# Performance work log

Measured on AMD Instinct MI355X. Metric: run time of the kernel, lower is better.

Reference implementation:

```python
import jax, jax.numpy as jnp
import numpy as np

B, T, V, C, H, HS, L, DFF = 8192, 8, 65, 512, 8, 64, 6, 2048
LN_EPS = 1e-5


def _layernorm(x, g, b):
    mu = jnp.mean(x, axis=-1, keepdims=True)
    var = jnp.mean(jnp.square(x - mu), axis=-1, keepdims=True)
    return (x - mu) * jax.lax.rsqrt(var + LN_EPS) * g + b


def setup_inputs() -> dict:
    key = jax.random.key(0)
    ks = jax.random.split(key, 16)
    s = 0.02
    inp = {
        "idx": jax.random.randint(ks[0], (B, T), 0, V),
        "tok_table": jax.random.normal(ks[1], (V, C), jnp.float32) * s,
        "pos_table": jax.random.normal(ks[2], (T, C), jnp.float32) * s,
        "wq": jax.random.normal(ks[3], (L, H, C, HS), jnp.float32) * s,
        "wk": jax.random.normal(ks[4], (L, H, C, HS), jnp.float32) * s,
        "wv": jax.random.normal(ks[5], (L, H, C, HS), jnp.float32) * s,
        "proj_w": jax.random.normal(ks[6], (L, C, C), jnp.float32) * s,
        "proj_b": jnp.zeros((L, C), jnp.float32),
        "w1": jax.random.normal(ks[7], (L, C, DFF), jnp.float32) * s,
        "b1": jnp.zeros((L, DFF), jnp.float32),
        "w2": jax.random.normal(ks[8], (L, DFF, C), jnp.float32) * s,
        "b2": jnp.zeros((L, C), jnp.float32),
        "ln1_g": jnp.ones((L, C), jnp.float32),
        "ln1_b": jnp.zeros((L, C), jnp.float32),
        "ln2_g": jnp.ones((L, C), jnp.float32),
        "ln2_b": jnp.zeros((L, C), jnp.float32),
        "lm_w": jax.random.normal(ks[9], (C, V), jnp.float32) * s,
        "lm_b": jnp.zeros((V,), jnp.float32),
    }
    return inp


def reference(idx, tok_table, pos_table, wq, wk, wv, proj_w, proj_b,
              w1, b1, w2, b2, ln1_g, ln1_b, ln2_g, ln2_b, lm_w, lm_b):
    idx = idx[:, -T:]
    x = tok_table[idx] + pos_table[None, :T, :]  # [B,T,C]
    mask = jnp.tril(jnp.ones((T, T), bool))
    scale = C ** (-0.5)  # NOTE: original scales by n_embed, not head_size
    for l in range(L):
        q = jnp.einsum('btc,hcd->bhtd', x, wq[l])
        k = jnp.einsum('btc,hcd->bhtd', x, wk[l])
        v = jnp.einsum('btc,hcd->bhtd', x, wv[l])
        att = jnp.einsum('bhtd,bhsd->bhts', q, k) * scale
        att = jnp.where(mask, att, -jnp.inf)
        att = jax.nn.softmax(att, axis=-1)
        o = jnp.einsum('bhts,bhsd->bhtd', att, v)
        o = o.transpose(0, 2, 1, 3).reshape(x.shape[0], T, C)  # concat heads
        o = o @ proj_w[l] + proj_b[l]
        x = _layernorm(x + o, ln1_g[l], ln1_b[l])  # post-norm
        h = jax.nn.relu(x @ w1[l] + b1[l]) @ w2[l] + b2[l]
        x = _layernorm(x + h, ln2_g[l], ln2_b[l])
    logits = x @ lm_w + lm_b  # [B,T,V]
    return logits
```

## Files before the change

### kernel.cpp

```cpp
#include <hip/hip_runtime.h>
#include <hip/hip_bf16.h>
#include <math.h>

#define NTOK  65536
#define CDIM  512
#define NHEAD 8
#define HSZ   64
#define NLAYER 6
#define DFF   2048
#define VOCAB 65

typedef unsigned short u16;
typedef __attribute__((ext_vector_type(8))) __bf16 bf16x8;
typedef __attribute__((ext_vector_type(4))) float f32x4;
typedef __attribute__((ext_vector_type(8))) unsigned short ushort8;

__device__ __forceinline__ float b2f(u16 u) {
    union { unsigned int i; float f; } x; x.i = ((unsigned int)u) << 16; return x.f;
}
__device__ __forceinline__ u16 f2b(float f) {
    union { float f; unsigned int i; } x; x.f = f;
    unsigned int r = x.i + 0x7fffu + ((x.i >> 16) & 1u);
    return (u16)(r >> 16);
}

__device__ __forceinline__ void async16(const u16* g, u16* l) {
    __builtin_amdgcn_global_load_lds(
        (const __attribute__((address_space(1))) void*)g,
        (__attribute__((address_space(3))) void*)l, 16, 0, 0);
}

template<int EPI>
__global__ __launch_bounds__(512)
void gemm_bt(const u16* __restrict__ A, const u16* __restrict__ Bt,
             void* __restrict__ Cout, const float* __restrict__ bias,
             const u16* __restrict__ res, int K, int N, int Nout)
{
    __shared__ u16 lA[2 * 256 * 32];
    __shared__ u16 lB[2 * 128 * 32];
    const int tid  = threadIdx.x;

    const int Nx = gridDim.x;
    const int id = blockIdx.y * Nx + blockIdx.x;
    const int xcd = id & 7;
    const int j0  = id >> 3;
    const int mt  = xcd + 8 * (j0 / Nx);
    const int nt  = j0 - (j0 / Nx) * Nx;
    const int m0  = mt * 256;
    const int n0  = nt * 128;

    const int lane = tid & 63;
    const int wv   = tid >> 6;
    const int wr   = (wv >> 1) * 64;
    const int wc   = (wv & 1) * 64;
    const int r16  = lane & 15;
    const int quad = lane >> 4;

    f32x4 acc[4][4] = {};

    const int srow = tid >> 2, skseg = (tid & 3) * 8;
    const u16* pA  = A  + (size_t)(m0 + srow) * K + skseg;
    const u16* pA2 = pA + (size_t)128 * K;
    const u16* pB  = Bt + (size_t)(n0 + srow) * K + skseg;
    u16* lAt = &lA[(size_t)tid * 8];
    u16* lBt = &lB[(size_t)tid * 8];

    async16(pA,  lAt);
    async16(pA2, lAt + 4096);
    async16(pB,  lBt);
    __syncthreads();

    int s = 0;
    for (int k0 = 0; k0 < K; k0 += 32) {
        if (k0 + 32 < K) {
            const int sn = (s ^ 1);
            async16(pA  + k0 + 32, lAt + sn * 8192);
            async16(pA2 + k0 + 32, lAt + sn * 8192 + 4096);
            async16(pB  + k0 + 32, lBt + sn * 4096);
        }
        const u16* bA = &lA[s * 8192];
        const u16* bB = &lB[s * 4096];
        bf16x8 af[4], bfr[4];
#pragma unroll
        for (int i = 0; i < 4; i++)
            af[i] = *(const bf16x8*)(const void*)&bA[(wr + i * 16 + r16) * 32 + quad * 8];
#pragma unroll
        for (int j = 0; j < 4; j++)
            bfr[j] = *(const bf16x8*)(const void*)&bB[(wc + j * 16 + r16) * 32 + quad * 8];
#pragma unroll
        for (int j = 0; j < 4; j++)
#pragma unroll
            for (int i = 0; i < 4; i++)
                acc[j][i] = __builtin_amdgcn_mfma_f32_16x16x32_bf16(bfr[j], af[i], acc[j][i], 0, 0, 0);
        __syncthreads();
        s ^= 1;
    }

#pragma unroll
    for (int i = 0; i < 4; i++) {
        const int row = m0 + wr + i * 16 + r16;
#pragma unroll
        for (int j = 0; j < 4; j++) {
            const int colb = n0 + wc + j * 16 + quad * 4;
            float v[4];
#pragma unroll
            for (int r = 0; r < 4; r++) v[r] = acc[j][i][r];
            if (EPI == 1 || EPI == 2) {
                const f32x4 b4 = *(const f32x4*)(const void*)&bias[colb];
#pragma unroll
                for (int r = 0; r < 4; r++) v[r] += b4[r];
            }
            if (EPI == 1) {
                const uint2 rv = *(const uint2*)(const void*)&res[(size_t)row * N + colb];
                v[0] += b2f((u16)(rv.x & 0xffffu));
                v[1] += b2f((u16)(rv.x >> 16));
                v[2] += b2f((u16)(rv.y & 0xffffu));
                v[3] += b2f((u16)(rv.y >> 16));
            }
            if (EPI == 2) {
#pragma unroll
                for (int r = 0; r < 4; r++) v[r] = fmaxf(v[r], 0.f);
            }
            if (EPI == 3) {
#pragma unroll
                for (int r = 0; r < 4; r++) {
                    const int col = colb + r;
                    if (col < Nout)
                        ((float*)Cout)[(size_t)row * Nout + col] = v[r] + bias[col];
                }
            } else {
                uint2 o;
                o.x = (unsigned)f2b(v[0]) | ((unsigned)f2b(v[1]) << 16);
                o.y = (unsigned)f2b(v[2]) | ((unsigned)f2b(v[3]) << 16);
                *(uint2*)(void*)&((u16*)Cout)[(size_t)row * N + colb] = o;
            }
        }
    }
}

__global__ __launch_bounds__(256)
void attn_k(const u16* __restrict__ qkv, u16* __restrict__ out)
{
    __shared__ float sq[4][8][64], sk[4][8][64], sv[4][8][64], sp[4][64];
    const int w = threadIdx.x >> 6, lane = threadIdx.x & 63;
    const int unit = blockIdx.x * 4 + w;
    const int b = unit >> 3, h = unit & 7;
    const size_t base = (size_t)b * 8 * 1536 + h * 64;
#pragma unroll
    for (int t = 0; t < 8; t++) {
        sq[w][t][lane] = b2f(qkv[base + t * 1536 + lane]);
        sk[w][t][lane] = b2f(qkv[base + t * 1536 + 512 + lane]);
        sv[w][t][lane] = b2f(qkv[base + t * 1536 + 1024 + lane]);
    }
    __syncthreads();
    const int t = lane >> 3, s = lane & 7;
    float sc = -1e30f;
    if (s <= t) {
        float d = 0.f;
#pragma unroll
        for (int c = 0; c < 64; c++) d += sq[w][t][c] * sk[w][s][c];
        sc = d * 0.04419417382415922f;
    }
    float mx = sc;
#pragma unroll
    for (int m = 1; m < 8; m <<= 1) mx = fmaxf(mx, __shfl_xor(mx, m, 8));
    float e = __expf(sc - mx);
    if (s > t) e = 0.f;
    float sum = e;
#pragma unroll
    for (int m = 1; m < 8; m <<= 1) sum += __shfl_xor(sum, m, 8);
    sp[w][lane] = e / sum;
    __syncthreads();
#pragma unroll
    for (int tt = 0; tt < 8; tt++) {
        float a = 0.f;
#pragma unroll
        for (int ss = 0; ss < 8; ss++) a += sp[w][tt * 8 + ss] * sv[w][ss][lane];
        out[((size_t)b * 8 + tt) * 512 + h * 64 + lane] = f2b(a);
    }
}

__global__ __launch_bounds__(256)
void ln_k(const u16* __restrict__ y, const float* __restrict__ g,
          const float* __restrict__ be, u16* __restrict__ x)
{
    const int w = threadIdx.x >> 6, lane = threadIdx.x & 63;
    const size_t tok = (size_t)blockIdx.x * 4 + w;
    const u16* row = y + tok * 512 + lane * 8;
    ushort8 raw = *(const ushort8*)(const void*)row;
    float v[8];
#pragma unroll
    for (int i = 0; i < 8; i++) v[i] = b2f(raw[i]);
    float s = 0.f;
#pragma unroll
    for (int i = 0; i < 8; i++) s += v[i];
#pragma unroll
    for (int m = 1; m < 64; m <<= 1) s += __shfl_xor(s, m, 64);
    const float mu = s * (1.f / 512.f);
    float q = 0.f;
#pragma unroll
    for (int i = 0; i < 8; i++) { float d = v[i] - mu; q += d * d; }
#pragma unroll
    for (int m = 1; m < 64; m <<= 1) q += __shfl_xor(q, m, 64);
    const float inv = rsqrtf(q * (1.f / 512.f) + 1e-5f);
    f32x4 g0  = *(const f32x4*)(const void*)&g[lane * 8];
    f32x4 g1  = *(const f32x4*)(const void*)&g[lane * 8 + 4];
    f32x4 b0  = *(const f32x4*)(const void*)&be[lane * 8];
    f32x4 b1v = *(const f32x4*)(const void*)&be[lane * 8 + 4];
    ushort8 o;
#pragma unroll
    for (int i = 0; i < 4; i++) o[i]     = f2b((v[i] - mu) * inv * g0[i] + b0[i]);
#pragma unroll
    for (int i = 0; i < 4; i++) o[i + 4] = f2b((v[i + 4] - mu) * inv * g1[i] + b1v[i]);
    *(ushort8*)(void*)&x[tok * 512 + lane * 8] = o;
}

__global__ __launch_bounds__(256)
void embed_k(const int* __restrict__ idx, const float* __restrict__ tokt,
             const float* __restrict__ pos, u16* __restrict__ xb)
{
    const int tk = blockIdx.x;
    const int t = tk & 7;
    const int ix = idx[tk];
    const int c = threadIdx.x;
    const size_t o = (size_t)tk * 512;
    xb[o + c]       = f2b(tokt[(size_t)ix * 512 + c]       + pos[t * 512 + c]);
    xb[o + c + 256] = f2b(tokt[(size_t)ix * 512 + c + 256] + pos[t * 512 + c + 256]);
}

__global__ __launch_bounds__(256)
void conv_t2_k(const float* __restrict__ in, u16* __restrict__ out, int K, int N)
{
    __shared__ float t[32][33];
    const int tx = threadIdx.x & 31, ty4 = (threadIdx.x >> 5) * 4;
    const int n0 = blockIdx.x * 32, k0 = blockIdx.y * 32, l = blockIdx.z;
    const size_t per = (size_t)K * N;
    const float* src = in + l * per;
#pragma unroll
    for (int r = 0; r < 4; r++)
        t[ty4 + r][tx] = src[(size_t)(k0 + ty4 + r) * N + n0 + tx];
    __syncthreads();
    u16* dst = out + l * per;
#pragma unroll
    for (int r = 0; r < 4; r++)
        dst[(size_t)(n0 + ty4 + r) * K + k0 + tx] = f2b(t[tx][ty4 + r]);
}

__global__ __launch_bounds__(256)
void conv_qkv2_k(const float* __restrict__ wq, const float* __restrict__ wk,
                 const float* __restrict__ wv, u16* __restrict__ out)
{
    __shared__ float t[32][33];
    const int tx = threadIdx.x & 31, ty4 = (threadIdx.x >> 5) * 4;
    const int c0 = blockIdx.x * 32, d0 = blockIdx.y * 32;
    const int z = blockIdx.z;
    const int sel = z / 48, rem = z - sel * 48;
    const int l = rem >> 3, h = rem & 7;
    const float* src = (sel == 0) ? wq : (sel == 1) ? wk : wv;
    const float* sb = src + (((size_t)l * 8 + h) * 512) * 64;
#pragma unroll
    for (int r = 0; r < 4; r++)
        t[ty4 + r][tx] = sb[(size_t)(c0 + ty4 + r) * 64 + d0 + tx];
    __syncthreads();
    u16* dst = out + (size_t)l * 786432 + (size_t)(sel * 512 + h * 64 + d0) * 512;
#pragma unroll
    for (int r = 0; r < 4; r++)
        dst[(size_t)(ty4 + r) * 512 + c0 + tx] = f2b(t[tx][ty4 + r]);
}

__global__ __launch_bounds__(256)
void conv_lm_k(const float* __restrict__ lm_w, u16* __restrict__ out)
{
    int gid = blockIdx.x * 256 + threadIdx.x;
    int n = gid >> 9, c = gid & 511;
    out[gid] = (n < VOCAB) ? f2b(lm_w[(size_t)c * VOCAB + n]) : (u16)0;
}

extern "C" void kernel_launch(void* const* d_in, const int* in_sizes, int n_in,
                              void* d_out, int out_size, void* d_ws, size_t ws_size,
                              hipStream_t stream)
{
    const int*   idx    = (const int*)  d_in[0];
    const float* tokt   = (const float*)d_in[1];
    const float* post   = (const float*)d_in[2];
    const float* wq     = (const float*)d_in[3];
    const float* wk     = (const float*)d_in[4];
    const float* wvp    = (const float*)d_in[5];
    const float* proj_w = (const float*)d_in[6];
    const float* proj_b = (const float*)d_in[7];
    const float* w1     = (const float*)d_in[8];
    const float* b1     = (const float*)d_in[9];
    const float* w2     = (const float*)d_in[10];
    const float* b2     = (const float*)d_in[11];
    const float* ln1_g  = (const float*)d_in[12];
    const float* ln1_b  = (const float*)d_in[13];
    const float* ln2_g  = (const float*)d_in[14];
    const float* ln2_b  = (const float*)d_in[15];
    const float* lm_w   = (const float*)d_in[16];
    const float* lm_b   = (const float*)d_in[17];
    float* out = (float*)d_out;

    char* ws = (char*)d_ws;
    u16* wqkvt = (u16*)(ws + 0);
    u16* wprjt = (u16*)(ws + 9437184);
    u16* ww1t  = (u16*)(ws + 12582912);
    u16* ww2t  = (u16*)(ws + 25165824);
    u16* wlmt  = (u16*)(ws + 37748736);
    u16* xb    = (u16*)(ws + 37879808);
    char* big  = ws + 104988672;

    const size_t fixed_bytes = 104988672ull;
    int chunk = 4096;
    const int cands[4] = {65536, 32768, 16384, 8192};
    for (int i = 0; i < 4; i++) {
        if (fixed_bytes + (size_t)cands[i] * 4096ull <= ws_size) { chunk = cands[i]; break; }
    }
    const int nchunks = NTOK / chunk;
    u16* qkvc  = (u16*)big;
    u16* attnc = (u16*)(big + (size_t)chunk * 3072);
    u16* h1c   = (u16*)big;

    conv_qkv2_k<<<dim3(16, 2, 144), 256, 0, stream>>>(wq, wk, wvp, wqkvt);
    conv_t2_k  <<<dim3(16, 16, 6), 256, 0, stream>>>(proj_w, wprjt, 512, 512);
    conv_t2_k  <<<dim3(64, 16, 6), 256, 0, stream>>>(w1, ww1t, 512, 2048);
    conv_t2_k  <<<dim3(16, 64, 6), 256, 0, stream>>>(w2, ww2t, 2048, 512);
    conv_lm_k  <<<128 * 512 / 256, 256, 0, stream>>>(lm_w, wlmt);

    embed_k<<<NTOK, 256, 0, stream>>>(idx, tokt, post, xb);

    for (int l = 0; l < NLAYER; l++) {
        for (int c = 0; c < nchunks; c++) {
            const size_t t0 = (size_t)c * chunk;
            gemm_bt<0><<<dim3(12, chunk / 256), 512, 0, stream>>>(
                xb + t0 * 512, wqkvt + (size_t)l * 786432, qkvc,
                nullptr, nullptr, 512, 1536, 1536);
            attn_k<<<chunk / 4, 256, 0, stream>>>(qkvc, attnc);
            gemm_bt<1><<<dim3(4, chunk / 256), 512, 0, stream>>>(
                attnc, wprjt + (size_t)l * 262144, xb + t0 * 512,
                proj_b + l * 512, xb + t0 * 512, 512, 512, 512);
        }
        ln_k<<<NTOK / 4, 256, 0, stream>>>(xb, ln1_g + l * 512, ln1_b + l * 512, xb);
        for (int c = 0; c < nchunks; c++) {
            const size_t t0 = (size_t)c * chunk;
            gemm_bt<2><<<dim3(16, chunk / 256), 512, 0, stream>>>(
                xb + t0 * 512, ww1t + (size_t)l * 1048576, h1c,
                b1 + l * 2048, nullptr, 512, 2048, 2048);
            gemm_bt<1><<<dim3(4, chunk / 256), 512, 0, stream>>>(
                h1c, ww2t + (size_t)l * 1048576, xb + t0 * 512,
                b2 + l * 512, xb + t0 * 512, 2048, 512, 512);
        }
        ln_k<<<NTOK / 4, 256, 0, stream>>>(xb, ln2_g + l * 512, ln2_b + l * 512, xb);
    }

    gemm_bt<3><<<dim3(1, 256), 512, 0, stream>>>(
        xb, wlmt, out, lm_b, nullptr, 512, 128, VOCAB);
}
```

Baseline: 4.468 ms.

## Fuse residual add and LayerNorm into full-row projection GEMM epilogue

Adds a gemm_ln kernel that computes a 128x512 full-row output tile so bias, residual add and LayerNorm can run in the epilogue with a cross-wave reduction through shared memory. This removes the separate ln_k passes and the extra round trip of the residual stream through global memory. The generic GEMM main loop also drops the double-buffered async prefetch in favour of loading 64-wide K chunks then computing, which removes overlap of loads with MFMA. LayerNorm variance now uses E[x^2]-mu^2 in fp32, which is slightly less numerically stable, and the wide tile uses many accumulator registers and yields fewer blocks.

```diff
diff --git a/kernel.cpp b/kernel.cpp
--- a/kernel.cpp
+++ b/kernel.cpp
@@ -34,7 +34,7 @@
 __global__ __launch_bounds__(512)
 void gemm_bt(const u16* __restrict__ A, const u16* __restrict__ Bt,
              void* __restrict__ Cout, const float* __restrict__ bias,
-             const u16* __restrict__ res, int K, int N, int Nout)
+             int K, int N, int Nout)
 {
     __shared__ u16 lA[2 * 256 * 32];
     __shared__ u16 lB[2 * 128 * 32];
@@ -65,35 +65,33 @@
     u16* lAt = &lA[(size_t)tid * 8];
     u16* lBt = &lB[(size_t)tid * 8];
 
-    async16(pA,  lAt);
-    async16(pA2, lAt + 4096);
-    async16(pB,  lBt);
-    __syncthreads();
-
-    int s = 0;
-    for (int k0 = 0; k0 < K; k0 += 32) {
-        if (k0 + 32 < K) {
-            const int sn = (s ^ 1);
-            async16(pA  + k0 + 32, lAt + sn * 8192);
-            async16(pA2 + k0 + 32, lAt + sn * 8192 + 4096);
-            async16(pB  + k0 + 32, lBt + sn * 4096);
-        }
-        const u16* bA = &lA[s * 8192];
-        const u16* bB = &lB[s * 4096];
-        bf16x8 af[4], bfr[4];
-#pragma unroll
-        for (int i = 0; i < 4; i++)
-            af[i] = *(const bf16x8*)(const void*)&bA[(wr + i * 16 + r16) * 32 + quad * 8];
-#pragma unroll
-        for (int j = 0; j < 4; j++)
-            bfr[j] = *(const bf16x8*)(const void*)&bB[(wc + j * 16 + r16) * 32 + quad * 8];
-#pragma unroll
-        for (int j = 0; j < 4; j++)
+    for (int k0 = 0; k0 < K; k0 += 64) {
+        async16(pA  + k0,      lAt);
+        async16(pA2 + k0,      lAt + 4096);
+        async16(pA  + k0 + 32, lAt + 8192);
+        async16(pA2 + k0 + 32, lAt + 12288);
+        async16(pB  + k0,      lBt);
+        async16(pB  + k0 + 32, lBt + 4096);
+        __syncthreads();
+
+#pragma unroll
+        for (int s = 0; s < 2; s++) {
+            const u16* bA = &lA[s * 8192];
+            const u16* bB = &lB[s * 4096];
+            bf16x8 af[4], bfr[4];
 #pragma unroll
             for (int i = 0; i < 4; i++)
-                acc[j][i] = __builtin_amdgcn_mfma_f32_16x16x32_bf16(bfr[j], af[i], acc[j][i], 0, 0, 0);
+                af[i] = *(const bf16x8*)(const void*)&bA[(wr + i * 16 + r16) * 32 + quad * 8];
+#pragma unroll
+            for (int j = 0; j < 4; j++)
+                bfr[j] = *(const bf16x8*)(const void*)&bB[(wc + j * 16 + r16) * 32 + quad * 8];
+#pragma unroll
+            for (int j = 0; j < 4; j++)
+#pragma unroll
+                for (int i = 0; i < 4; i++)
+                    acc[j][i] = __builtin_amdgcn_mfma_f32_16x16x32_bf16(bfr[j], af[i], acc[j][i], 0, 0, 0);
+        }
         __syncthreads();
-        s ^= 1;
     }
 
 #pragma unroll
@@ -105,21 +103,10 @@
             float v[4];
 #pragma unroll
             for (int r = 0; r < 4; r++) v[r] = acc[j][i][r];
-            if (EPI == 1 || EPI == 2) {
+            if (EPI == 2) {
                 const f32x4 b4 = *(const f32x4*)(const void*)&bias[colb];
 #pragma unroll
-                for (int r = 0; r < 4; r++) v[r] += b4[r];
-            }
-            if (EPI == 1) {
-                const uint2 rv = *(const uint2*)(const void*)&res[(size_t)row * N + colb];
-                v[0] += b2f((u16)(rv.x & 0xffffu));
-                v[1] += b2f((u16)(rv.x >> 16));
-                v[2] += b2f((u16)(rv.y & 0xffffu));
-                v[3] += b2f((u16)(rv.y >> 16));
-            }
-            if (EPI == 2) {
-#pragma unroll
-                for (int r = 0; r < 4; r++) v[r] = fmaxf(v[r], 0.f);
+                for (int r = 0; r < 4; r++) v[r] = fmaxf(v[r] + b4[r], 0.f);
             }
             if (EPI == 3) {
 #pragma unroll
@@ -138,6 +125,127 @@
     }
 }
 
+__global__ __launch_bounds__(512, 2)
+void gemm_ln(const u16* __restrict__ A, const u16* __restrict__ Bt,
+             const float* __restrict__ bias, const u16* __restrict__ res,
+             const float* __restrict__ g, const float* __restrict__ be,
+             u16* __restrict__ X, int K)
+{
+    __shared__ u16 lA[2 * 128 * 32];
+    __shared__ u16 lB[2 * 512 * 32];
+    __shared__ float rsum[128][4];
+    __shared__ float rsq[128][4];
+    const int tid  = threadIdx.x;
+    const int m0   = blockIdx.x * 128;
+    const int lane = tid & 63;
+    const int wv   = tid >> 6;
+    const int wrow = (wv >> 2) * 64;
+    const int wcol = (wv & 3) * 128;
+    const int cg   = wv & 3;
+    const int r16  = lane & 15;
+    const int quad = lane >> 4;
+
+    f32x4 acc[8][4] = {};
+
+    const int arow = tid >> 2, aseg = (tid & 3) * 8;
+    const u16* pA = A  + (size_t)(m0 + arow) * K + aseg;
+    const u16* pB = Bt + (size_t)arow * K + aseg;
+    const size_t bK128 = (size_t)128 * K;
+    u16* lAt = &lA[(size_t)tid * 8];
+    u16* lBt = &lB[(size_t)tid * 8];
+
+    for (int k0 = 0; k0 < K; k0 += 64) {
+        async16(pA + k0,      lAt);
+        async16(pA + k0 + 32, lAt + 4096);
+#pragma unroll
+        for (int i = 0; i < 4; i++) {
+            async16(pB + i * bK128 + k0,      lBt + i * 4096);
+            async16(pB + i * bK128 + k0 + 32, lBt + 16384 + i * 4096);
+        }
+        __syncthreads();
+
+#pragma unroll
+        for (int s = 0; s < 2; s++) {
+            const u16* bA = &lA[s * 4096];
+            const u16* bB = &lB[s * 16384];
+            bf16x8 af[4], bfr[8];
+#pragma unroll
+            for (int i = 0; i < 4; i++)
+                af[i] = *(const bf16x8*)(const void*)&bA[(wrow + i * 16 + r16) * 32 + quad * 8];
+#pragma unroll
+            for (int j = 0; j < 8; j++)
+                bfr[j] = *(const bf16x8*)(const void*)&bB[(wcol + j * 16 + r16) * 32 + quad * 8];
+#pragma unroll
+            for (int j = 0; j < 8; j++)
+#pragma unroll
+                for (int i = 0; i < 4; i++)
+                    acc[j][i] = __builtin_amdgcn_mfma_f32_16x16x32_bf16(bfr[j], af[i], acc[j][i], 0, 0, 0);
+        }
+        __syncthreads();
+    }
+
+    float ps[4] = {0.f, 0.f, 0.f, 0.f}, pq[4] = {0.f, 0.f, 0.f, 0.f};
+#pragma unroll
+    for (int j = 0; j < 8; j++) {
+        const int colb = wcol + j * 16 + quad * 4;
+        const f32x4 b4 = *(const f32x4*)(const void*)&bias[colb];
+#pragma unroll
+        for (int i = 0; i < 4; i++) {
+            const int row = m0 + wrow + i * 16 + r16;
+            const uint2 rv = *(const uint2*)(const void*)&res[(size_t)row * 512 + colb];
+            float v0 = acc[j][i][0] + b4[0] + b2f((u16)(rv.x & 0xffffu));
+            float v1 = acc[j][i][1] + b4[1] + b2f((u16)(rv.x >> 16));
+            float v2 = acc[j][i][2] + b4[2] + b2f((u16)(rv.y & 0xffffu));
+            float v3 = acc[j][i][3] + b4[3] + b2f((u16)(rv.y >> 16));
+            acc[j][i][0] = v0; acc[j][i][1] = v1;
+            acc[j][i][2] = v2; acc[j][i][3] = v3;
+            ps[i] += (v0 + v1) + (v2 + v3);
+            pq[i] += (v0 * v0 + v1 * v1) + (v2 * v2 + v3 * v3);
+        }
+    }
+#pragma unroll
+    for (int i = 0; i < 4; i++) {
+        ps[i] += __shfl_xor(ps[i], 16); ps[i] += __shfl_xor(ps[i], 32);
+        pq[i] += __shfl_xor(pq[i], 16); pq[i] += __shfl_xor(pq[i], 32);
+    }
+    if (quad == 0) {
+#pragma unroll
+        for (int i = 0; i < 4; i++) {
+            rsum[wrow + i * 16 + r16][cg] = ps[i];
+            rsq [wrow + i * 16 + r16][cg] = pq[i];
+        }
+    }
+    __syncthreads();
+    float mu[4], rstd[4];
+#pragma unroll
+    for (int i = 0; i < 4; i++) {
+        const int lr = wrow + i * 16 + r16;
+        const float s = (rsum[lr][0] + rsum[lr][1]) + (rsum[lr][2] + rsum[lr][3]);
+        const float q = (rsq[lr][0] + rsq[lr][1]) + (rsq[lr][2] + rsq[lr][3]);
+        mu[i] = s * (1.f / 512.f);
+        const float var = q * (1.f / 512.f) - mu[i] * mu[i];
+        rstd[i] = rsqrtf(var + 1e-5f);
+    }
+#pragma unroll
+    for (int j = 0; j < 8; j++) {
+        const int colb = wcol + j * 16 + quad * 4;
+        const f32x4 g4 = *(const f32x4*)(const void*)&g[colb];
+        const f32x4 e4 = *(const f32x4*)(const void*)&be[colb];
+#pragma unroll
+        for (int i = 0; i < 4; i++) {
+            const int row = m0 + wrow + i * 16 + r16;
+            const float v0 = (acc[j][i][0] - mu[i]) * rstd[i] * g4[0] + e4[0];
+            const float v1 = (acc[j][i][1] - mu[i]) * rstd[i] * g4[1] + e4[1];
+            const float v2 = (acc[j][i][2] - mu[i]) * rstd[i] * g4[2] + e4[2];
+            const float v3 = (acc[j][i][3] - mu[i]) * rstd[i] * g4[3] + e4[3];
+            uint2 o;
+            o.x = (unsigned)f2b(v0) | ((unsigned)f2b(v1) << 16);
+            o.y = (unsigned)f2b(v2) | ((unsigned)f2b(v3) << 16);
+            *(uint2*)(void*)&X[(size_t)row * 512 + colb] = o;
+        }
+    }
+}
+
 __global__ __launch_bounds__(256)
 void attn_k(const u16* __restrict__ qkv, u16* __restrict__ out)
 {
@@ -178,41 +286,6 @@
         for (int ss = 0; ss < 8; ss++) a += sp[w][tt * 8 + ss] * sv[w][ss][lane];
         out[((size_t)b * 8 + tt) * 512 + h * 64 + lane] = f2b(a);
     }
-}
-
-__global__ __launch_bounds__(256)
-void ln_k(const u16* __restrict__ y, const float* __restrict__ g,
-          const float* __restrict__ be, u16* __restrict__ x)
-{
-    const int w = threadIdx.x >> 6, lane = threadIdx.x & 63;
-    const size_t tok = (size_t)blockIdx.x * 4 + w;
-    const u16* row = y + tok * 512 + lane * 8;
-    ushort8 raw = *(const ushort8*)(const void*)row;
-    float v[8];
-#pragma unroll
-    for (int i = 0; i < 8; i++) v[i] = b2f(raw[i]);
-    float s = 0.f;
-#pragma unroll
-    for (int i = 0; i < 8; i++) s += v[i];
-#pragma unroll
-    for (int m = 1; m < 64; m <<= 1) s += __shfl_xor(s, m, 64);
-    const float mu = s * (1.f / 512.f);
-    float q = 0.f;
-#pragma unroll
-    for (int i = 0; i < 8; i++) { float d = v[i] - mu; q += d * d; }
-#pragma unroll
-    for (int m = 1; m < 64; m <<= 1) q += __shfl_xor(q, m, 64);
-    const float inv = rsqrtf(q * (1.f / 512.f) + 1e-5f);
-    f32x4 g0  = *(const f32x4*)(const void*)&g[lane * 8];
-    f32x4 g1  = *(const f32x4*)(const void*)&g[lane * 8 + 4];
-    f32x4 b0  = *(const f32x4*)(const void*)&be[lane * 8];
-    f32x4 b1v = *(const f32x4*)(const void*)&be[lane * 8 + 4];
-    ushort8 o;
-#pragma unroll
-    for (int i = 0; i < 4; i++) o[i]     = f2b((v[i] - mu) * inv * g0[i] + b0[i]);
-#pragma unroll
-    for (int i = 0; i < 4; i++) o[i + 4] = f2b((v[i + 4] - mu) * inv * g1[i] + b1v[i]);
-    *(ushort8*)(void*)&x[tok * 512 + lane * 8] = o;
 }
 
 __global__ __launch_bounds__(256)
@@ -333,25 +406,25 @@
             const size_t t0 = (size_t)c * chunk;
             gemm_bt<0><<<dim3(12, chunk / 256), 512, 0, stream>>>(
                 xb + t0 * 512, wqkvt + (size_t)l * 786432, qkvc,
-                nullptr, nullptr, 512, 1536, 1536);
+                nullptr, 512, 1536, 1536);
             attn_k<<<chunk / 4, 256, 0, stream>>>(qkvc, attnc);
-            gemm_bt<1><<<dim3(4, chunk / 256), 512, 0, stream>>>(
-                attnc, wprjt + (size_t)l * 262144, xb + t0 * 512,
-                proj_b + l * 512, xb + t0 * 512, 512, 512, 512);
-        }
-        ln_k<<<NTOK / 4, 256, 0, stream>>>(xb, ln1_g + l * 512, ln1_b + l * 512, xb);
+            gemm_ln<<<dim3(chunk / 128), 512, 0, stream>>>(
+                attnc, wprjt + (size_t)l * 262144, proj_b + l * 512,
+                xb + t0 * 512, ln1_g + l * 512, ln1_b + l * 512,
+                xb + t0 * 512, 512);
+        }
         for (int c = 0; c < nchunks; c++) {
             const size_t t0 = (size_t)c * chunk;
             gemm_bt<2><<<dim3(16, chunk / 256), 512, 0, stream>>>(
                 xb + t0 * 512, ww1t + (size_t)l * 1048576, h1c,
-                b1 + l * 2048, nullptr, 512, 2048, 2048);
-            gemm_bt<1><<<dim3(4, chunk / 256), 512, 0, stream>>>(
-                h1c, ww2t + (size_t)l * 1048576, xb + t0 * 512,
-                b2 + l * 512, xb + t0 * 512, 2048, 512, 512);
-        }
-        ln_k<<<NTOK / 4, 256, 0, stream>>>(xb, ln2_g + l * 512, ln2_b + l * 512, xb);
+                b1 + l * 2048, 512, 2048, 2048);
+            gemm_ln<<<dim3(chunk / 128), 512, 0, stream>>>(
+                h1c, ww2t + (size_t)l * 1048576, b2 + l * 512,
+                xb + t0 * 512, ln2_g + l * 512, ln2_b + l * 512,
+                xb + t0 * 512, 2048);
+        }
     }
 
     gemm_bt<3><<<dim3(1, 256), 512, 0, stream>>>(
-        xb, wlmt, out, lm_b, nullptr, 512, 128, VOCAB);
-}
+        xb, wlmt, out, lm_b, 512, 128, VOCAB);
+}
```

Result: no change. 4.512 ms (+1.0%).
